# Kernel tuning notes

Measured on AMD Instinct MI355X. Metric: run time of the kernel, lower is better.

Reference implementation:

```python
import jax, jax.numpy as jnp
import numpy as np

NUM_HEADS = 8
TEMPERATURE = 10000.0


def sine_embed(pos, dim):
    """Sine positional embedding of 2D offsets. pos [..., 2] -> [..., dim]."""
    half = dim // 2  # dims per coordinate
    dim_t = TEMPERATURE ** (2.0 * (jnp.arange(half) // 2).astype(jnp.float32) / half)
    s = pos[..., :, None] / dim_t  # [..., 2, half]
    emb = jnp.stack([jnp.sin(s[..., 0::2]), jnp.cos(s[..., 1::2])], axis=-1)
    emb = emb.reshape(s.shape[:-1] + (half,))  # interleaved sin/cos per coord
    return emb.reshape(pos.shape[:-1] + (dim,))


def setup_inputs() -> dict:
    key = jax.random.key(0)
    ks = jax.random.split(key, 16)
    N, H, W, C, K = 2, 40, 40, 256, 100
    h = NUM_HEADS
    sc = 1.0 / np.sqrt(C)
    return {
        "query_feature": jax.random.normal(ks[0], (N, H, W, C), jnp.float32),
        "query_position": jax.random.uniform(ks[1], (N, H, W, 2), jnp.float32),
        "key_feature": jax.random.normal(ks[2], (N, K, C), jnp.float32),
        "key_position": jax.random.uniform(ks[3], (N, K, 2), jnp.float32),
        # MultiheadAttention params (torch convention: weight [out, in])
        "in_proj_w": jax.random.normal(ks[4], (3 * C, C), jnp.float32) * sc,
        "in_proj_b": jnp.zeros((3 * C,), jnp.float32),
        "out_proj_w": jax.random.normal(ks[5], (C, C), jnp.float32) * sc,
        "out_proj_b": jnp.zeros((C,), jnp.float32),
        # PositionalEncodingSineLearned MLP: sine(C) -> C -> num_heads
        "pos_w1": jax.random.normal(ks[6], (C, C), jnp.float32) * sc,
        "pos_b1": jnp.zeros((C,), jnp.float32),
        "pos_w2": jax.random.normal(ks[7], (h, C), jnp.float32) * sc,
        "pos_b2": jnp.zeros((h,), jnp.float32),
        # cat_pos branch params
        "pos_trans_w": jax.random.normal(ks[8], (2, 2), jnp.float32),
        "embed_w": jax.random.normal(ks[9], (C, C + 2), jnp.float32) * 0.01,
        "embed_b": jnp.zeros((C,), jnp.float32),
    }


def reference(query_feature, query_position, key_feature, key_position,
              in_proj_w, in_proj_b, out_proj_w, out_proj_b,
              pos_w1, pos_b1, pos_w2, pos_b2,
              pos_trans_w, embed_w, embed_b):
    N, H, W, C = query_feature.shape
    h = NUM_HEADS
    d = C // h
    q = query_feature.reshape(N, -1, C)            # [N,Q,C]
    qp = query_position.reshape(N, -1, 2)          # [N,Q,2] (scale_terms = 1.0)
    Q = q.shape[1]
    K = key_feature.shape[1]

    # pairwise relative positions: [N,Q,K,2]
    rel_pos = key_position[:, None, :, :] - qp[:, :, None, :]

    # learned sine relative positional encoding -> per-head additive bias
    pe = sine_embed(rel_pos, C)                              # [N,Q,K,C]
    hid = jax.nn.relu(pe @ pos_w1.T + pos_b1)                # [N,Q,K,C]
    bias = (hid @ pos_w2.T + pos_b2).transpose(0, 3, 1, 2)   # [N,h,Q,K]

    # multihead attention with additive relative bias
    wq, wk, wv = jnp.split(in_proj_w, 3, axis=0)
    bq, bk, bv = jnp.split(in_proj_b, 3, axis=0)
    qh = ((q @ wq.T + bq).reshape(N, Q, h, d)) * (d ** -0.5)
    kh = (key_feature @ wk.T + bk).reshape(N, K, h, d)
    vh = (key_feature @ wv.T + bv).reshape(N, K, h, d)
    scores = jnp.einsum('nqhd,nkhd->nhqk', qh, kh) + bias
    attn = jax.nn.softmax(scores, axis=-1)                   # [N,h,Q,K]
    ctx = jnp.einsum('nhqk,nkhd->nqhd', attn, vh).reshape(N, Q, C)
    refined = ctx @ out_proj_w.T + out_proj_b                # [N,Q,C]

    # cat_pos: attention-weighted relative position aggregation
    attn_w = attn.mean(axis=1)                               # [N,Q,K]
    new_rel = jnp.einsum('nqk,nqkc->nqc', attn_w, jax.lax.stop_gradient(rel_pos))
    new_pos = new_rel @ pos_trans_w.T                        # [N,Q,2]

    feat = jax.nn.relu(q + refined)
    feat = jax.nn.relu(jnp.concatenate([feat, new_pos], axis=-1) @ embed_w.T + embed_b)
    return feat.reshape(N, H, W, C)
```

## Files before the change

kernel.cpp:

```cpp
#include <hip/hip_runtime.h>
#include <math.h>

typedef __bf16 bf16x8 __attribute__((ext_vector_type(8)));
typedef __bf16 bf16x4 __attribute__((ext_vector_type(4)));
typedef float  f32x4  __attribute__((ext_vector_type(4)));


#define WS_KH    0u
#define WS_VH    51200u
#define WS_EWP   102400u
#define WS_QHB   168960u
#define WS_BIASB 578560u
#define WS_KEB   2012160u
#define WS_W1B   2038560u
#define WS_W2PB  2071328u
#define WS_QEB   2073376u

__device__ __forceinline__ float rdlane(float v, int l) {
  return __uint_as_float(__builtin_amdgcn_readlane(__float_as_uint(v), l));
}

__device__ __forceinline__ unsigned packbf(float a, float b) {
  unsigned short ua = __builtin_bit_cast(unsigned short, (__bf16)a);
  unsigned short ub = __builtin_bit_cast(unsigned short, (__bf16)b);
  return (unsigned)ua | ((unsigned)ub << 16);
}

__global__ __launch_bounds__(256, 2) void prep_kernel(
    const float* __restrict__ qfeat, const float* __restrict__ kfeat,
    const float* __restrict__ kpos, const float* __restrict__ qpos,
    const float* __restrict__ ipw, const float* __restrict__ ipb,
    const float* __restrict__ pos_w1, const float* __restrict__ pos_w2,
    const float* __restrict__ embed_w, float* __restrict__ ws)
{
  __shared__ float x[8 * 256];
  int bid = blockIdx.x, t = threadIdx.x;

  if (bid < 50) {
    int r = bid * 4 + (t >> 6);
    int u = t & 63;
    float p0 = kpos[r * 2 + 0], p1 = kpos[r * 2 + 1];
    __bf16* keb = (__bf16*)(ws + WS_KEB);
    bf16x4 o;
#pragma unroll
    for (int j = 0; j < 4; j++) {
      int col = u * 4 + j;
      int c = col >> 7, i = (col & 127) >> 1;
      float p = c ? p1 : p0;
      float inv = exp2f((float)i * (-13.287712379549449f / 64.0f));
      float v = p * inv;
      o[j] = (__bf16)((col & 1) ? __cosf(v) : __sinf(v));
    }
    *(bf16x4*)(keb + r * 264 + u * 4) = o;
  } else if (bid < 114) {
    int idx = (bid - 50) * 1024 + t * 4;
    float4 v = *(const float4*)(pos_w1 + idx);
    bf16x4 o; o[0] = (__bf16)v.x; o[1] = (__bf16)v.y; o[2] = (__bf16)v.z; o[3] = (__bf16)v.w;
    *(bf16x4*)((__bf16*)(ws + WS_W1B) + idx) = o;
  } else if (bid == 114) {
    __bf16* w2pb = (__bf16*)(ws + WS_W2PB);
    for (int i = 0; i < 16; i++) {
      int idx = t * 16 + i;
      w2pb[idx] = (idx < 2048) ? (__bf16)pos_w2[idx] : (__bf16)0.0f;
    }
  } else if (bid < 147) {
    int r0 = (bid - 115) * 8;
    for (int rr = 0; rr < 8; rr++) {
      int r = r0 + rr;
      for (int j = t; j < 260; j += 256)
        ws[WS_EWP + r * 260 + j] = (j < 258) ? embed_w[r * 258 + j] : 0.0f;
    }
  } else if (bid < 547) {
    int r0 = (bid - 147) * 8;
    for (int i = t; i < 2048; i += 256) x[i] = qfeat[(unsigned)r0 * 256u + i];
    __syncthreads();
    float acc[8]; float bq = ipb[t];
#pragma unroll
    for (int rr = 0; rr < 8; rr++) acc[rr] = bq;
    const float* wrow = ipw + (unsigned)t * 256u;
    for (int j = 0; j < 256; j += 4) {
      float4 w4 = *(const float4*)(wrow + j);
#pragma unroll
      for (int rr = 0; rr < 8; rr++) {
        float4 x4 = *(const float4*)(x + rr * 256 + j);
        acc[rr] = fmaf(x4.x, w4.x, fmaf(x4.y, w4.y, fmaf(x4.z, w4.z, fmaf(x4.w, w4.w, acc[rr]))));
      }
    }
    __bf16* qhb = (__bf16*)(ws + WS_QHB);
#pragma unroll
    for (int rr = 0; rr < 8; rr++)
      qhb[(unsigned)(r0 + rr) * 256u + t] = (__bf16)(acc[rr] * 0.17677669529663687f);
  } else if (bid < 579) {
    int b2 = bid - 547; int n = b2 >> 4, tile = b2 & 15;
    int r0l = tile * 7; int cnt = 100 - r0l; if (cnt > 7) cnt = 7; if (cnt <= 0) return;
    int r0 = n * 100 + r0l;
    for (int i = t; i < cnt * 256; i += 256) x[i] = kfeat[(unsigned)r0 * 256u + i];
    __syncthreads();
    float ak[7], av[7]; float bk = ipb[256 + t], bv = ipb[512 + t];
#pragma unroll
    for (int rr = 0; rr < 7; rr++) { ak[rr] = bk; av[rr] = bv; }
    const float* wkr = ipw + (unsigned)(256 + t) * 256u;
    const float* wvr = ipw + (unsigned)(512 + t) * 256u;
    for (int j = 0; j < 256; j += 4) {
      float4 wk4 = *(const float4*)(wkr + j);
      float4 wv4 = *(const float4*)(wvr + j);
#pragma unroll
      for (int rr = 0; rr < 7; rr++) {
        float4 x4 = *(const float4*)(x + rr * 256 + j);
        ak[rr] = fmaf(x4.x, wk4.x, fmaf(x4.y, wk4.y, fmaf(x4.z, wk4.z, fmaf(x4.w, wk4.w, ak[rr]))));
        av[rr] = fmaf(x4.x, wv4.x, fmaf(x4.y, wv4.y, fmaf(x4.z, wv4.z, fmaf(x4.w, wv4.w, av[rr]))));
      }
    }
    for (int rr = 0; rr < 7; rr++) {
      if (rr < cnt) {
        ws[WS_KH + (unsigned)(r0 + rr) * 256u + t] = ak[rr];
        ws[WS_VH + (unsigned)(r0 + rr) * 256u + t] = av[rr];
      }
    }
  } else {
    int r = (bid - 579) * 4 + (t >> 6);
    int u = t & 63;
    float p0 = qpos[r * 2 + 0], p1 = qpos[r * 2 + 1];
    __bf16* qeb = (__bf16*)(ws + WS_QEB);
    bf16x4 o;
#pragma unroll
    for (int j = 0; j < 4; j++) {
      int col = u * 4 + j;
      int c = col >> 7, i = (col & 127) >> 1;
      float p = c ? p1 : p0;
      float inv = exp2f((float)i * (-13.287712379549449f / 64.0f));
      float v = p * inv;
      o[j] = (__bf16)((col & 1) ? __cosf(v) : __sinf(v));
    }
    *(bf16x4*)(qeb + r * 256 + u * 4) = o;
  }
}

__global__ __launch_bounds__(512, 2) void bias_kernel(
    const float* __restrict__ pos_b1, const float* __restrict__ pos_b2,
    float* __restrict__ ws)
{
  __shared__ __align__(16) char qe_smem[32768];
  __shared__ __align__(16) char hid_smem[32768];
  __shared__ __align__(16) __bf16 keb_s[256];

  int bid = blockIdx.x;
  int nk = bid / 5, g = bid - nk * 5;
  int n = nk / 100, k = nk - n * 100;
  int qbase = n * 1600 + g * 320;
  int t = threadIdx.x;
  int lane = t & 63, w = t >> 6;
  int wc = w & 3, wq = w >> 2;
  int l15 = lane & 15, quad = lane >> 4;

  const __bf16* keb = (const __bf16*)(ws + WS_KEB) + (unsigned)nk * 264u;
  const __bf16* qeb = (const __bf16*)(ws + WS_QEB);
  const __bf16* w1b = (const __bf16*)(ws + WS_W1B);
  const __bf16* w2pb = (const __bf16*)(ws + WS_W2PB);
  __bf16* biasb = (__bf16*)(ws + WS_BIASB);

  if (t < 32) *(bf16x8*)(keb_s + t * 8) = *(const bf16x8*)(keb + t * 8);

  int sr = t >> 3, ssub = t & 7, sswz = (sr & 7) << 4;
  {
    const __bf16* src = qeb + (unsigned)(qbase + sr) * 256u + ssub * 32;
    char* dst = qe_smem + sr * 512;
#pragma unroll
    for (int u = 0; u < 4; u++) {
      bf16x8 v = *(const bf16x8*)(src + u * 8);
      *(bf16x8*)(dst + ((ssub * 64 + u * 16) ^ sswz)) = v;
    }
  }

  int xm = (l15 & 7) << 4;
  int colx[8];
#pragma unroll
  for (int kc = 0; kc < 8; kc++) colx[kc] = ((kc * 64 + quad * 16) ^ xm);
  const __bf16* w1p = w1b + (unsigned)(wc * 64 + l15) * 256u + quad * 8;

  float b1a[4][4];
#pragma unroll
  for (int ct = 0; ct < 4; ct++)
#pragma unroll
    for (int r = 0; r < 4; r++) b1a[ct][r] = pos_b1[wc * 64 + ct * 16 + quad * 4 + r];

  f32x4 zero4; zero4[0] = 0.f; zero4[1] = 0.f; zero4[2] = 0.f; zero4[3] = 0.f;

  __syncthreads();

  bf16x8 af[8][4];
#pragma unroll
  for (int kc = 0; kc < 8; kc++) {
    bf16x8 ke8 = *(const bf16x8*)(keb_s + kc * 32 + quad * 8);
#pragma unroll
    for (int ct = 0; ct < 4; ct++) {
      bf16x8 w8 = *(const bf16x8*)(w1p + ct * 4096 + kc * 32);
      bf16x8 a;
#pragma unroll
      for (int p2 = 0; p2 < 4; p2++) {
        float we = (float)w8[2 * p2], wo = (float)w8[2 * p2 + 1];
        float sk = (float)ke8[2 * p2], ck = (float)ke8[2 * p2 + 1];
        a[2 * p2]     = (__bf16)fmaf(wo, sk, -(we * ck));
        a[2 * p2 + 1] = (__bf16)fmaf(we, sk, wo * ck);
      }
      af[kc][ct] = a;
    }
  }

#pragma unroll 1
  for (int tt = 0; tt < 5; tt++) {
    bf16x8 qv[4];
    if (tt < 4) {
      const __bf16* src = qeb + (unsigned)(qbase + (tt + 1) * 64 + sr) * 256u + ssub * 32;
#pragma unroll
      for (int u = 0; u < 4; u++) qv[u] = *(const bf16x8*)(src + u * 8);
    }

    f32x4 acc[4][2];
#pragma unroll
    for (int ct = 0; ct < 4; ct++)
#pragma unroll
      for (int nt = 0; nt < 2; nt++) acc[ct][nt] = zero4;

#pragma unroll
    for (int kc = 0; kc < 8; kc++) {
#pragma unroll
      for (int nt = 0; nt < 2; nt++) {
        int row = wq * 32 + nt * 16 + l15;
        bf16x8 qf = *(const bf16x8*)(qe_smem + row * 512 + colx[kc]);
        acc[0][nt] = __builtin_amdgcn_mfma_f32_16x16x32_bf16(af[kc][0], qf, acc[0][nt], 0, 0, 0);
        acc[1][nt] = __builtin_amdgcn_mfma_f32_16x16x32_bf16(af[kc][1], qf, acc[1][nt], 0, 0, 0);
        acc[2][nt] = __builtin_amdgcn_mfma_f32_16x16x32_bf16(af[kc][2], qf, acc[2][nt], 0, 0, 0);
        acc[3][nt] = __builtin_amdgcn_mfma_f32_16x16x32_bf16(af[kc][3], qf, acc[3][nt], 0, 0, 0);
      }
    }

#pragma unroll
    for (int ct = 0; ct < 4; ct++) {
#pragma unroll
      for (int nt = 0; nt < 2; nt++) {
        int q = wq * 32 + nt * 16 + l15;
        unsigned lo = packbf(fmaxf(acc[ct][nt][0] + b1a[ct][0], 0.f),
                             fmaxf(acc[ct][nt][1] + b1a[ct][1], 0.f));
        unsigned hi = packbf(fmaxf(acc[ct][nt][2] + b1a[ct][2], 0.f),
                             fmaxf(acc[ct][nt][3] + b1a[ct][3], 0.f));
        int cbyte = wc * 128 + ct * 32 + quad * 8;
        char* p = hid_smem + q * 512 + (cbyte ^ ((q & 7) << 4));
        unsigned long long v = (unsigned long long)lo | ((unsigned long long)hi << 32);
        *(unsigned long long*)p = v;
      }
    }

    __syncthreads();

    if (tt < 4) {
      char* dst = qe_smem + sr * 512;
#pragma unroll
      for (int u = 0; u < 4; u++)
        *(bf16x8*)(dst + ((ssub * 64 + u * 16) ^ sswz)) = qv[u];
    }

    if (wq == 0) {
      bf16x8 w2f[8];
#pragma unroll
      for (int kc = 0; kc < 8; kc++)
        w2f[kc] = *(const bf16x8*)(w2pb + (unsigned)l15 * 256u + kc * 32 + quad * 8);
      int row = wc * 16 + l15;
      const char* hbase = hid_smem + row * 512;
      int hxm = (l15 & 7) << 4;
      f32x4 acc2 = zero4;
#pragma unroll
      for (int kc = 0; kc < 8; kc++) {
        bf16x8 hf = *(const bf16x8*)(hbase + ((kc * 64 + quad * 16) ^ hxm));
        acc2 = __builtin_amdgcn_mfma_f32_16x16x32_bf16(w2f[kc], hf, acc2, 0, 0, 0);
      }
      if (quad < 2) {
        int qg = qbase + tt * 64 + row;
        bf16x4 o;
#pragma unroll
        for (int r = 0; r < 4; r++) o[r] = (__bf16)(acc2[r] + pos_b2[quad * 4 + r]);
        *(bf16x4*)(biasb + (unsigned)qg * 896u + (unsigned)k * 8u + quad * 4) = o;
      }
    }

    if (tt < 4) __syncthreads();
  }
}

__global__ __launch_bounds__(256, 4) void attn_kernel(
    const float* __restrict__ qfeat, const float* __restrict__ qpos,
    const float* __restrict__ kpos,
    const float* __restrict__ out_w, const float* __restrict__ out_b,
    const float* __restrict__ embed_b, const float* __restrict__ ptw,
    const float* __restrict__ ws, float* __restrict__ out)
{
  __shared__ float qh_s[4 * 8 * 36];
  __shared__ float attn_s[4 * 8 * 116];
  __shared__ float ctx_s[4 * 264];
  __shared__ float cat_s[4 * 264];
  __shared__ float aw_s[4 * 104];

  int bid = blockIdx.x;
  int qg0 = bid * 4;
  int n = bid / 400;
  int t = threadIdx.x;

  const __bf16* qhb = (const __bf16*)(ws + WS_QHB);
  const __bf16* biasb = (const __bf16*)(ws + WS_BIASB);
  const float* kh = ws + WS_KH;
  const float* vh = ws + WS_VH;
  const float* ewp = ws + WS_EWP;

  for (int i = t; i < 1024; i += 256) {
    int q = i >> 8, c = i & 255;
    qh_s[(q * 8 + (c >> 5)) * 36 + (c & 31)] = (float)qhb[(unsigned)(qg0 + q) * 256u + c];
  }
  __syncthreads();

  for (int i = 0; i < 4; i++) {
    int p = t + i * 256;
    if (p < 800) {
      int k = p >> 3, h = p & 7;
      const float4* kf = (const float4*)(kh + (unsigned)(n * 100 + k) * 256u + h * 32);
      float4 kv[8];
#pragma unroll
      for (int dd = 0; dd < 8; dd++) kv[dd] = kf[dd];
#pragma unroll
      for (int q = 0; q < 4; q++) {
        const float4* qf = (const float4*)(qh_s + (q * 8 + h) * 36);
        float s = (float)biasb[((unsigned)(qg0 + q) * 112u + k) * 8u + h];
#pragma unroll
        for (int dd = 0; dd < 8; dd++) {
          float4 qv = qf[dd];
          s += kv[dd].x * qv.x + kv[dd].y * qv.y + kv[dd].z * qv.z + kv[dd].w * qv.w;
        }
        attn_s[(q * 8 + h) * 116 + k] = s;
      }
    }
  }
  __syncthreads();

  {
    int q = t >> 6, h = (t >> 3) & 7, j = t & 7;
    float* row = attn_s + (q * 8 + h) * 116;
    float mx = -1e30f;
    for (int k = j; k < 100; k += 8) mx = fmaxf(mx, row[k]);
    mx = fmaxf(mx, __shfl_xor(mx, 1, 8));
    mx = fmaxf(mx, __shfl_xor(mx, 2, 8));
    mx = fmaxf(mx, __shfl_xor(mx, 4, 8));
    float sum = 0.f;
    for (int k = j; k < 100; k += 8) { float e = __expf(row[k] - mx); row[k] = e; sum += e; }
    sum += __shfl_xor(sum, 1, 8);
    sum += __shfl_xor(sum, 2, 8);
    sum += __shfl_xor(sum, 4, 8);
    float inv = 1.0f / sum;
    for (int k = j; k < 100; k += 8) row[k] *= inv;
  }
  __syncthreads();

  for (int p = t; p < 416; p += 256) {
    int q = p / 104, k = p % 104;
    if (k < 100) {
      float s = 0.f;
#pragma unroll
      for (int h = 0; h < 8; h++) s += attn_s[(q * 8 + h) * 116 + k];
      aw_s[q * 104 + k] = s * 0.125f;
    }
  }
  {
    int c = t, h = c >> 5;
    float a0 = 0.f, a1 = 0.f, a2 = 0.f, a3 = 0.f;
    const float* vp = vh + (unsigned)(n * 100) * 256u + c;
    const float* r0 = attn_s + (0 * 8 + h) * 116;
    const float* r1 = attn_s + (1 * 8 + h) * 116;
    const float* r2 = attn_s + (2 * 8 + h) * 116;
    const float* r3 = attn_s + (3 * 8 + h) * 116;
#pragma unroll 4
    for (int k = 0; k < 100; k++) {
      float vv = vp[(unsigned)k * 256u];
      a0 = fmaf(r0[k], vv, a0);
      a1 = fmaf(r1[k], vv, a1);
      a2 = fmaf(r2[k], vv, a2);
      a3 = fmaf(r3[k], vv, a3);
    }
    ctx_s[0 * 264 + c] = a0; ctx_s[1 * 264 + c] = a1;
    ctx_s[2 * 264 + c] = a2; ctx_s[3 * 264 + c] = a3;
  }
  __syncthreads();

  if (t < 8) {
    int q = t >> 1, cd = t & 1;
    float qp = qpos[(qg0 + q) * 2 + cd];
    float s = 0.f;
    for (int k = 0; k < 100; k++)
      s = fmaf(aw_s[q * 104 + k], kpos[(n * 100 + k) * 2 + cd] - qp, s);
    float so = __shfl_xor(s, 1, 2);
    if (cd == 0) cat_s[q * 264 + 256] = ptw[0] * s + ptw[1] * so;
    else         cat_s[q * 264 + 257] = ptw[2] * so + ptw[3] * s;
  }

  {
    int c = t, lane = t & 63;
    float ob = out_b[c];
    float acc0 = ob, acc1 = ob, acc2 = ob, acc3 = ob;
    const float* wr = out_w + (unsigned)c * 256u;
    for (int ch = 0; ch < 4; ch++) {
      float v0 = ctx_s[0 * 264 + ch * 64 + lane];
      float v1 = ctx_s[1 * 264 + ch * 64 + lane];
      float v2 = ctx_s[2 * 264 + ch * 64 + lane];
      float v3 = ctx_s[3 * 264 + ch * 64 + lane];
      const float* wp = wr + ch * 64;
#pragma unroll 4
      for (int j4 = 0; j4 < 16; j4++) {
        float4 w4 = *(const float4*)(wp + j4 * 4);
        int jb = j4 * 4;
        acc0 = fmaf(rdlane(v0, jb + 0), w4.x, acc0);
        acc1 = fmaf(rdlane(v1, jb + 0), w4.x, acc1);
        acc2 = fmaf(rdlane(v2, jb + 0), w4.x, acc2);
        acc3 = fmaf(rdlane(v3, jb + 0), w4.x, acc3);
        acc0 = fmaf(rdlane(v0, jb + 1), w4.y, acc0);
        acc1 = fmaf(rdlane(v1, jb + 1), w4.y, acc1);
        acc2 = fmaf(rdlane(v2, jb + 1), w4.y, acc2);
        acc3 = fmaf(rdlane(v3, jb + 1), w4.y, acc3);
        acc0 = fmaf(rdlane(v0, jb + 2), w4.z, acc0);
        acc1 = fmaf(rdlane(v1, jb + 2), w4.z, acc1);
        acc2 = fmaf(rdlane(v2, jb + 2), w4.z, acc2);
        acc3 = fmaf(rdlane(v3, jb + 2), w4.z, acc3);
        acc0 = fmaf(rdlane(v0, jb + 3), w4.w, acc0);
        acc1 = fmaf(rdlane(v1, jb + 3), w4.w, acc1);
        acc2 = fmaf(rdlane(v2, jb + 3), w4.w, acc2);
        acc3 = fmaf(rdlane(v3, jb + 3), w4.w, acc3);
      }
    }
    cat_s[0 * 264 + c] = fmaxf(qfeat[(unsigned)(qg0 + 0) * 256u + c] + acc0, 0.f);
    cat_s[1 * 264 + c] = fmaxf(qfeat[(unsigned)(qg0 + 1) * 256u + c] + acc1, 0.f);
    cat_s[2 * 264 + c] = fmaxf(qfeat[(unsigned)(qg0 + 2) * 256u + c] + acc2, 0.f);
    cat_s[3 * 264 + c] = fmaxf(qfeat[(unsigned)(qg0 + 3) * 256u + c] + acc3, 0.f);
  }
  __syncthreads();

  {
    int c = t, lane = t & 63;
    float eb = embed_b[c];
    float acc0 = eb, acc1 = eb, acc2 = eb, acc3 = eb;
    const float* er = ewp + (unsigned)c * 260u;
    for (int ch = 0; ch < 4; ch++) {
      float v0 = cat_s[0 * 264 + ch * 64 + lane];
      float v1 = cat_s[1 * 264 + ch * 64 + lane];
      float v2 = cat_s[2 * 264 + ch * 64 + lane];
      float v3 = cat_s[3 * 264 + ch * 64 + lane];
      const float* wp = er + ch * 64;
#pragma unroll 4
      for (int j4 = 0; j4 < 16; j4++) {
        float4 w4 = *(const float4*)(wp + j4 * 4);
        int jb = j4 * 4;
        acc0 = fmaf(rdlane(v0, jb + 0), w4.x, acc0);
        acc1 = fmaf(rdlane(v1, jb + 0), w4.x, acc1);
        acc2 = fmaf(rdlane(v2, jb + 0), w4.x, acc2);
        acc3 = fmaf(rdlane(v3, jb + 0), w4.x, acc3);
        acc0 = fmaf(rdlane(v0, jb + 1), w4.y, acc0);
        acc1 = fmaf(rdlane(v1, jb + 1), w4.y, acc1);
        acc2 = fmaf(rdlane(v2, jb + 1), w4.y, acc2);
        acc3 = fmaf(rdlane(v3, jb + 1), w4.y, acc3);
        acc0 = fmaf(rdlane(v0, jb + 2), w4.z, acc0);
        acc1 = fmaf(rdlane(v1, jb + 2), w4.z, acc1);
        acc2 = fmaf(rdlane(v2, jb + 2), w4.z, acc2);
        acc3 = fmaf(rdlane(v3, jb + 2), w4.z, acc3);
        acc0 = fmaf(rdlane(v0, jb + 3), w4.w, acc0);
        acc1 = fmaf(rdlane(v1, jb + 3), w4.w, acc1);
        acc2 = fmaf(rdlane(v2, jb + 3), w4.w, acc2);
        acc3 = fmaf(rdlane(v3, jb + 3), w4.w, acc3);
      }
    }
    float4 wt = *(const float4*)(er + 256);
    acc0 += cat_s[0 * 264 + 256] * wt.x + cat_s[0 * 264 + 257] * wt.y;
    acc1 += cat_s[1 * 264 + 256] * wt.x + cat_s[1 * 264 + 257] * wt.y;
    acc2 += cat_s[2 * 264 + 256] * wt.x + cat_s[2 * 264 + 257] * wt.y;
    acc3 += cat_s[3 * 264 + 256] * wt.x + cat_s[3 * 264 + 257] * wt.y;
    out[(unsigned)(qg0 + 0) * 256u + c] = fmaxf(acc0, 0.f);
    out[(unsigned)(qg0 + 1) * 256u + c] = fmaxf(acc1, 0.f);
    out[(unsigned)(qg0 + 2) * 256u + c] = fmaxf(acc2, 0.f);
    out[(unsigned)(qg0 + 3) * 256u + c] = fmaxf(acc3, 0.f);
  }
}

extern "C" void kernel_launch(void* const* d_in, const int* in_sizes, int n_in,
                              void* d_out, int out_size, void* d_ws, size_t ws_size,
                              hipStream_t stream)
{
  const float* query_feature  = (const float*)d_in[0];
  const float* query_position = (const float*)d_in[1];
  const float* key_feature    = (const float*)d_in[2];
  const float* key_position   = (const float*)d_in[3];
  const float* in_proj_w      = (const float*)d_in[4];
  const float* in_proj_b      = (const float*)d_in[5];
  const float* out_proj_w     = (const float*)d_in[6];
  const float* out_proj_b     = (const float*)d_in[7];
  const float* pos_w1         = (const float*)d_in[8];
  const float* pos_b1         = (const float*)d_in[9];
  const float* pos_w2         = (const float*)d_in[10];
  const float* pos_b2         = (const float*)d_in[11];
  const float* pos_trans_w    = (const float*)d_in[12];
  const float* embed_w        = (const float*)d_in[13];
  const float* embed_b        = (const float*)d_in[14];
  float* ws  = (float*)d_ws;
  float* out = (float*)d_out;

  hipLaunchKernelGGL(prep_kernel, dim3(1379), dim3(256), 0, stream,
                     query_feature, key_feature, key_position, query_position,
                     in_proj_w, in_proj_b, pos_w1, pos_w2, embed_w, ws);
  hipLaunchKernelGGL(bias_kernel, dim3(1000), dim3(512), 0, stream,
                     pos_b1, pos_b2, ws);
  hipLaunchKernelGGL(attn_kernel, dim3(800), dim3(256), 0, stream,
                     query_feature, query_position, key_position,
                     out_proj_w, out_proj_b, embed_b, pos_trans_w,
                     ws, out);
}
```

Before: 275.6 us.

## Double-buffer bias kernel smem and defer second GEMM one tile

The bias kernel's query-embedding and hidden-activation shared buffers are double-buffered. The second small GEMM (hidden to per-head bias) for tile t-1 is now computed at the start of iteration t, overlapping the next tile's first GEMM, which cuts one barrier per iteration. The bias stores are collected in registers and written once at the end. Shared memory grows from about 64KB to 128KB per block, which may lower occupancy below the two blocks per CU requested in the launch bounds.

New measurement: 271.3 us. About the same (-1.5%).

```diff
diff --git a/kernel.cpp b/kernel.cpp
--- a/kernel.cpp
+++ b/kernel.cpp
@@ -140,8 +140,8 @@
     const float* __restrict__ pos_b1, const float* __restrict__ pos_b2,
     float* __restrict__ ws)
 {
-  __shared__ __align__(16) char qe_smem[32768];
-  __shared__ __align__(16) char hid_smem[32768];
+  __shared__ __align__(16) char qe_smem[2][32768];
+  __shared__ __align__(16) char hid_smem[2][32768];
   __shared__ __align__(16) __bf16 keb_s[256];
 
   int bid = blockIdx.x;
@@ -164,7 +164,7 @@
   int sr = t >> 3, ssub = t & 7, sswz = (sr & 7) << 4;
   {
     const __bf16* src = qeb + (unsigned)(qbase + sr) * 256u + ssub * 32;
-    char* dst = qe_smem + sr * 512;
+    char* dst = qe_smem[0] + sr * 512;
 #pragma unroll
     for (int u = 0; u < 4; u++) {
       bf16x8 v = *(const bf16x8*)(src + u * 8);
@@ -183,6 +183,9 @@
   for (int ct = 0; ct < 4; ct++)
 #pragma unroll
     for (int r = 0; r < 4; r++) b1a[ct][r] = pos_b1[wc * 64 + ct * 16 + quad * 4 + r];
+  float b2v[4];
+#pragma unroll
+  for (int r = 0; r < 4; r++) b2v[r] = pos_b2[(quad * 4 + r) & 7];
 
   f32x4 zero4; zero4[0] = 0.f; zero4[1] = 0.f; zero4[2] = 0.f; zero4[3] = 0.f;
 
@@ -207,7 +210,28 @@
     }
   }
 
-#pragma unroll 1
+  unsigned long long bias_pk[5];
+
+  auto gemm2 = [&](int tg) {
+    bf16x8 w2f[8];
+#pragma unroll
+    for (int kc = 0; kc < 8; kc++)
+      w2f[kc] = *(const bf16x8*)(w2pb + (unsigned)l15 * 256u + kc * 32 + quad * 8);
+    int row = wc * 16 + l15;
+    const char* hbase = hid_smem[tg & 1] + row * 512;
+    int hxm = (l15 & 7) << 4;
+    f32x4 acc2 = zero4;
+#pragma unroll
+    for (int kc = 0; kc < 8; kc++) {
+      bf16x8 hf = *(const bf16x8*)(hbase + ((kc * 64 + quad * 16) ^ hxm));
+      acc2 = __builtin_amdgcn_mfma_f32_16x16x32_bf16(w2f[kc], hf, acc2, 0, 0, 0);
+    }
+    unsigned lo = packbf(acc2[0] + b2v[0], acc2[1] + b2v[1]);
+    unsigned hi = packbf(acc2[2] + b2v[2], acc2[3] + b2v[3]);
+    return (unsigned long long)lo | ((unsigned long long)hi << 32);
+  };
+
+#pragma unroll
   for (int tt = 0; tt < 5; tt++) {
     bf16x8 qv[4];
     if (tt < 4) {
@@ -216,6 +240,8 @@
       for (int u = 0; u < 4; u++) qv[u] = *(const bf16x8*)(src + u * 8);
     }
 
+    if (tt > 0 && wq == 0) bias_pk[tt - 1] = gemm2(tt - 1);
+
     f32x4 acc[4][2];
 #pragma unroll
     for (int ct = 0; ct < 4; ct++)
@@ -227,7 +253,7 @@
 #pragma unroll
       for (int nt = 0; nt < 2; nt++) {
         int row = wq * 32 + nt * 16 + l15;
-        bf16x8 qf = *(const bf16x8*)(qe_smem + row * 512 + colx[kc]);
+        bf16x8 qf = *(const bf16x8*)(qe_smem[tt & 1] + row * 512 + colx[kc]);
         acc[0][nt] = __builtin_amdgcn_mfma_f32_16x16x32_bf16(af[kc][0], qf, acc[0][nt], 0, 0, 0);
         acc[1][nt] = __builtin_amdgcn_mfma_f32_16x16x32_bf16(af[kc][1], qf, acc[1][nt], 0, 0, 0);
         acc[2][nt] = __builtin_amdgcn_mfma_f32_16x16x32_bf16(af[kc][2], qf, acc[2][nt], 0, 0, 0);
@@ -245,45 +271,32 @@
         unsigned hi = packbf(fmaxf(acc[ct][nt][2] + b1a[ct][2], 0.f),
                              fmaxf(acc[ct][nt][3] + b1a[ct][3], 0.f));
         int cbyte = wc * 128 + ct * 32 + quad * 8;
-        char* p = hid_smem + q * 512 + (cbyte ^ ((q & 7) << 4));
-        unsigned long long v = (unsigned long long)lo | ((unsigned long long)hi << 32);
-        *(unsigned long long*)p = v;
-      }
-    }
-
-    __syncthreads();
+        char* p = hid_smem[tt & 1] + q * 512 + (cbyte ^ ((q & 7) << 4));
+        *(unsigned long long*)p = (unsigned long long)lo | ((unsigned long long)hi << 32);
+      }
+    }
 
     if (tt < 4) {
-      char* dst = qe_smem + sr * 512;
+      char* dst = qe_smem[(tt + 1) & 1] + sr * 512;
 #pragma unroll
       for (int u = 0; u < 4; u++)
         *(bf16x8*)(dst + ((ssub * 64 + u * 16) ^ sswz)) = qv[u];
     }
 
-    if (wq == 0) {
-      bf16x8 w2f[8];
-#pragma unroll
-      for (int kc = 0; kc < 8; kc++)
-        w2f[kc] = *(const bf16x8*)(w2pb + (unsigned)l15 * 256u + kc * 32 + quad * 8);
+    __syncthreads();
+  }
+
+  if (wq == 0) {
+    bias_pk[4] = gemm2(4);
+    if (quad < 2) {
       int row = wc * 16 + l15;
-      const char* hbase = hid_smem + row * 512;
-      int hxm = (l15 & 7) << 4;
-      f32x4 acc2 = zero4;
-#pragma unroll
-      for (int kc = 0; kc < 8; kc++) {
-        bf16x8 hf = *(const bf16x8*)(hbase + ((kc * 64 + quad * 16) ^ hxm));
-        acc2 = __builtin_amdgcn_mfma_f32_16x16x32_bf16(w2f[kc], hf, acc2, 0, 0, 0);
-      }
-      if (quad < 2) {
-        int qg = qbase + tt * 64 + row;
-        bf16x4 o;
-#pragma unroll
-        for (int r = 0; r < 4; r++) o[r] = (__bf16)(acc2[r] + pos_b2[quad * 4 + r]);
-        *(bf16x4*)(biasb + (unsigned)qg * 896u + (unsigned)k * 8u + quad * 4) = o;
-      }
-    }
-
-    if (tt < 4) __syncthreads();
+#pragma unroll
+      for (int tg = 0; tg < 5; tg++) {
+        int qg = qbase + tg * 64 + row;
+        *(unsigned long long*)(biasb + (unsigned)qg * 896u + (unsigned)k * 8u + quad * 4)
+            = bias_pk[tg];
+      }
+    }
   }
 }
 
```
